# Kernel tuning notes

Measured on AMD Instinct MI355X. Metric: run time of the kernel, lower is better.

## Reference

```python
import jax, jax.numpy as jnp
import numpy as np

B, CIN, COUT, H, W = 4, 256, 256, 64, 64
K, G = 3, 4
PAD = (K - 1) // 2


def setup_inputs() -> dict:
    key = jax.random.key(0)
    k0, k1, k2, k3 = jax.random.split(key, 4)
    x = jax.random.normal(k0, (B, CIN, H, W), jnp.float32)
    y = jax.random.normal(k1, (B, 2, H, W), jnp.float32)
    # conv_offset: 1x1 conv, no bias, init std=0.1 (normal_init)
    w_offset = jax.random.normal(k2, (G * 2 * K * K, 2, 1, 1), jnp.float32) * 0.1
    # DeformConv2d weight, no bias, init std=0.01
    w_deform = jax.random.normal(k3, (COUT, CIN, K, K), jnp.float32) * 0.01
    return {"x": x, "y": y, "w_offset": w_offset, "w_deform": w_deform}


def _deform_conv(x, offset, weight):
    """DCN v1: stride 1, dilation 1, zero padding PAD, deform_groups=G, groups=1."""
    KK = K * K
    # mmcv offset layout: [B, G*2*KK, H, W] -> per group, per kernel pos, (dy, dx)
    off = offset.reshape(B, G, KK, 2, H, W)
    dy, dx = off[:, :, :, 0], off[:, :, :, 1]            # [B,G,KK,H,W]
    ii, jj = jnp.meshgrid(jnp.arange(K), jnp.arange(K), indexing="ij")
    ky = ii.reshape(KK).astype(x.dtype)                  # kernel row offsets
    kx = jj.reshape(KK).astype(x.dtype)                  # kernel col offsets
    base_y = jnp.arange(H, dtype=x.dtype)[None, :, None] - PAD + ky[:, None, None]  # [KK,H,1]
    base_x = jnp.arange(W, dtype=x.dtype)[None, None, :] - PAD + kx[:, None, None]  # [KK,1,W]
    yc = dy + base_y                                     # [B,G,KK,H,W]
    xc = dx + base_x

    Cg = CIN // G
    xg = x.reshape(B, G, Cg, H, W)

    def sample(xg1, yc1, xc1):
        # xg1 [Cg,H,W]; yc1/xc1 [KK,H,W] -> bilinear sample with zero padding
        y0 = jnp.floor(yc1)
        x0 = jnp.floor(xc1)
        wy = yc1 - y0
        wx = xc1 - x0
        y0i = y0.astype(jnp.int32)
        x0i = x0.astype(jnp.int32)

        def gather(yi, xi):
            valid = (yi >= 0) & (yi < H) & (xi >= 0) & (xi < W)
            v = xg1[:, jnp.clip(yi, 0, H - 1), jnp.clip(xi, 0, W - 1)]  # [Cg,KK,H,W]
            return v * valid[None].astype(xg1.dtype)

        v00 = gather(y0i, x0i)
        v01 = gather(y0i, x0i + 1)
        v10 = gather(y0i + 1, x0i)
        v11 = gather(y0i + 1, x0i + 1)
        return (v00 * (1 - wy) * (1 - wx) + v01 * (1 - wy) * wx
                + v10 * wy * (1 - wx) + v11 * wy * wx)

    sampled = jax.vmap(jax.vmap(sample))(xg, yc, xc)     # [B,G,Cg,KK,H,W]
    sampled = sampled.reshape(B, CIN, KK, H, W)
    wflat = weight.reshape(COUT, CIN, KK)
    return jnp.einsum("bckhw,ock->bohw", sampled, wflat)  # [B,COUT,H,W]


def reference(x, y, w_offset, w_deform):
    # offset = conv_offset(y.detach()), a 1x1 conv without bias
    y_det = jax.lax.stop_gradient(y)
    offset = jnp.einsum("bihw,oi->bohw", y_det, w_offset[:, :, 0, 0])
    out = _deform_conv(x, offset, w_deform)
    return jax.nn.relu(out)
```

## Files before the change

### kernel.cpp

```cpp
#include <hip/hip_runtime.h>
#include <cstddef>

#define B_    4
#define CIN_  256
#define COUT_ 256
#define H_    64
#define W_    64
#define KK_   9
#define G_    4
#define NSL   36
#define PW    80
#define PH    80
#define PADO  8

typedef short bf16x8 __attribute__((ext_vector_type(8)));
typedef float f32x4  __attribute__((ext_vector_type(4)));
typedef __attribute__((address_space(1))) const unsigned int* gptr_t;
typedef __attribute__((address_space(3))) unsigned int*       lptr_t;

__device__ __forceinline__ unsigned short f2bf(float v) {
    unsigned int u = __float_as_uint(v);
    u += 0x7fffu + ((u >> 16) & 1u);
    return (unsigned short)(u >> 16);
}
__device__ __forceinline__ float f_lo(unsigned int u) { return __uint_as_float(u << 16); }
__device__ __forceinline__ float f_hi(unsigned int u) { return __uint_as_float(u & 0xffff0000u); }

__global__ __launch_bounds__(256) void prep_kernel(const float* __restrict__ x,
                                                   unsigned short* __restrict__ xTp,
                                                   const float* __restrict__ w,
                                                   unsigned short* __restrict__ wb) {
    const int tid = threadIdx.x;
    if (blockIdx.x < 512) {
        __shared__ unsigned short s[128][66];
        const int bh    = blockIdx.x >> 1;
        const int chalf = blockIdx.x & 1;
        const int b     = bh >> 6, h = bh & 63;
        const size_t src_base = ((size_t)b * CIN_ + chalf * 128) * (H_ * W_) + h * W_;
        #pragma unroll 4
        for (int k = 0; k < 32; ++k) {
            int i = k * 256 + tid;
            int c = i >> 6, ww = i & 63;
            s[c][ww] = f2bf(x[src_base + (size_t)c * (H_ * W_) + ww]);
        }
        __syncthreads();
        const size_t dst_row = ((size_t)b * PH + (h + PADO)) * PW;
        #pragma unroll 4
        for (int k = 0; k < 20; ++k) {
            int j  = k * 256 + tid;
            int c2 = (j & 63) * 2, wp = j >> 6;
            unsigned int v = 0;
            if (wp >= PADO && wp < PADO + W_) {
                int ww = wp - PADO;
                v = (unsigned int)s[c2][ww] | ((unsigned int)s[c2 + 1][ww] << 16);
            }
            *(unsigned int*)(xTp + (dst_row + wp) * 256 + chalf * 128 + c2) = v;
        }
    } else if (blockIdx.x < 576) {
        const int bidx = blockIdx.x - 512;
        const int b = bidx >> 4, rr = bidx & 15;
        const int yp = (rr < PADO) ? rr : (PH - 16 + rr);
        unsigned short* dst = xTp + ((size_t)b * PH + yp) * PW * 256;
        #pragma unroll
        for (int k = 0; k < 10; ++k) {
            *(uint4*)(dst + (size_t)(k * 256 + tid) * 8) = make_uint4(0, 0, 0, 0);
        }
    } else {
        int idx = (blockIdx.x - 576) * 256 + tid;
        int e   = idx & 7;
        int pos = (idx >> 3) & 7;
        int o   = (idx >> 6) & 255;
        int t   = idx >> 14;
        int g   = t / 9, kk = t - g * 9;
        int j   = pos ^ (o & 7);
        int c   = g * 64 + j * 8 + e;
        wb[idx] = f2bf(w[(o * CIN_ + c) * KK_ + kk]);
    }
}

__global__ __launch_bounds__(1024, 4) void dcn_kernel(
    const unsigned short* __restrict__ xTp, const float* __restrict__ y,
    const float* __restrict__ w_off, const unsigned short* __restrict__ wb,
    float* __restrict__ out)
{
    __shared__ unsigned short s_W[3][COUT_ * 64];
    __shared__ unsigned short s_S[2][64 * 64];

    const int tid = threadIdx.x;
    const int bid = blockIdx.x;
    const int xcd = bid & 7;
    const int b   = xcd >> 1;
    const int h   = (xcd & 1) * 32 + (bid >> 3);

    const int sp = tid >> 4;
    const int c4 = tid & 15;

    const float yv0 = y[((b * 2 + 0) * H_ + h) * W_ + sp];
    const float yv1 = y[((b * 2 + 1) * H_ + h) * W_ + sp];
    const float spf = (float)(sp - 1 + PADO);
    const float hpf = (float)(h - 1 + PADO);

    const int lane = tid & 63, wave = tid >> 6;
    const int pg  = wave & 1, oh = wave >> 1;
    const int l15 = lane & 15, kq = lane >> 4, sw = l15 & 7;

    f32x4 acc[4];
    #pragma unroll
    for (int i = 0; i < 4; ++i) acc[i] = (f32x4){0.f, 0.f, 0.f, 0.f};

    const unsigned short* xb = xTp + (size_t)b * (PH * PW * 256) + c4 * 4;

    float w00, w01, w10, w11;
    uint2 A, Bv, C, D;

#define ISSUE_SAMPLE(t) do {                                                   \
    const int g_ = (t) / 9, kk_ = (t) % 9;                                     \
    const float4 co = *(const float4*)(w_off + (t) * 4);                       \
    const float dy = fmaf(yv0, co.x, yv1 * co.y);                              \
    const float dx = fmaf(yv0, co.z, yv1 * co.w);                              \
    const float yc = hpf + (float)(kk_ / 3) + dy;                              \
    const float xc = spf + (float)(kk_ % 3) + dx;                              \
    const float yf = floorf(yc), xf = floorf(xc);                              \
    const float wy = yc - yf,    wx = xc - xf;                                 \
    const int   yi = (int)yf,    xi = (int)xf;         \
    const float omy = 1.f - wy,  omx = 1.f - wx;                               \
    w00 = omy * omx;  w01 = omy * wx;                                          \
    w10 = wy * omx;   w11 = wy * wx;                                           \
    const int idx0 = (yi * PW + xi) * 256 + g_ * 64;               \
    A  = *(const uint2*)(xb + idx0);                                           \
    Bv = *(const uint2*)(xb + idx0 + 256);                 \
    C  = *(const uint2*)(xb + idx0 + PW * 256);                       \
    D  = *(const uint2*)(xb + idx0 + PW * 256 + 256);                          \
} while (0)

#define STAGE_W(t, buf) do {                                                   \
    const unsigned short* src = wb + (size_t)(t) * 16384;                      \
    _Pragma("unroll")                                                          \
    for (int j = 0; j < 2; ++j) {                                              \
        const int off = (j * 1024 + tid) * 8;                                  \
        __builtin_amdgcn_global_load_lds((gptr_t)(src + off),                  \
                                         (lptr_t)(s_W[buf] + off), 16, 0, 2); \
    }                                                                          \
} while (0)

#define WRITE_SAMPLE(buf) do {                                                 \
    float r0 = w00 * f_lo(A.x);                                                \
    r0 = fmaf(w01, f_lo(Bv.x), r0);                                            \
    r0 = fmaf(w10, f_lo(C.x),  r0);                                            \
    r0 = fmaf(w11, f_lo(D.x),  r0);                                            \
    float r1 = w00 * f_hi(A.x);                                                \
    r1 = fmaf(w01, f_hi(Bv.x), r1);                                            \
    r1 = fmaf(w10, f_hi(C.x),  r1);                                            \
    r1 = fmaf(w11, f_hi(D.x),  r1);                                            \
    float r2 = w00 * f_lo(A.y);                                                \
    r2 = fmaf(w01, f_lo(Bv.y), r2);                                            \
    r2 = fmaf(w10, f_lo(C.y),  r2);                                            \
    r2 = fmaf(w11, f_lo(D.y),  r2);                                            \
    float r3 = w00 * f_hi(A.y);                                                \
    r3 = fmaf(w01, f_hi(Bv.y), r3);                                            \
    r3 = fmaf(w10, f_hi(C.y),  r3);                                            \
    r3 = fmaf(w11, f_hi(D.y),  r3);                                            \
    unsigned int res0 = __builtin_amdgcn_perm(__float_as_uint(r1),             \
                                __float_as_uint(r0), 0x07060302u);             \
    unsigned int res1 = __builtin_amdgcn_perm(__float_as_uint(r3),             \
                                __float_as_uint(r2), 0x07060302u);             \
    *(uint2*)(s_S[buf] + sp * 64 + (((c4 >> 1) ^ (sp & 7)) * 8) +              \
              (c4 & 1) * 4) = make_uint2(res0, res1);                          \
} while (0)

#define MFMA_STEP(wb_, sb_) do {                                               \
    bf16x8 bf[2][2], af[2][2];                                                 \
    _Pragma("unroll")                                                          \
    for (int kh = 0; kh < 2; ++kh) {                                           \
        const int pos = ((kh * 4 + kq) ^ sw) * 8;                              \
        _Pragma("unroll")                                                      \
        for (int nt = 0; nt < 2; ++nt)                                         \
            bf[kh][nt] = *(const bf16x8*)(s_S[sb_] +                           \
                              (pg * 32 + nt * 16 + l15) * 64 + pos);           \
        _Pragma("unroll")                                                      \
        for (int mt = 0; mt < 2; ++mt)                                         \
            af[kh][mt] = *(const bf16x8*)(s_W[wb_] +                           \
                              (oh * 32 + mt * 16 + l15) * 64 + pos);           \
    }                                                                          \
    __builtin_amdgcn_s_setprio(1);                                             \
    _Pragma("unroll")                                                          \
    for (int kh = 0; kh < 2; ++kh)                                             \
        _Pragma("unroll")                                                      \
        for (int nt = 0; nt < 2; ++nt)                                         \
            _Pragma("unroll")                                                  \
            for (int mt = 0; mt < 2; ++mt)                                     \
                acc[nt * 2 + mt] = __builtin_amdgcn_mfma_f32_16x16x32_bf16(    \
                    af[kh][mt], bf[kh][nt], acc[nt * 2 + mt], 0, 0, 0);        \
    __builtin_amdgcn_s_setprio(0);                                             \
} while (0)

#define STEP(s_, WCUR, WPRE, SCUR, SNXT, DO_ISS, DO_STG, DO_BAR) do {          \
    if (DO_ISS) ISSUE_SAMPLE((s_) + 1);                                        \
    __builtin_amdgcn_sched_barrier(0);                                         \
    if (DO_STG) STAGE_W((s_) + 2, WPRE);                                       \
    __builtin_amdgcn_sched_barrier(0);                                         \
    MFMA_STEP(WCUR, SCUR);                                                     \
    __builtin_amdgcn_sched_barrier(0);                                         \
    if (DO_ISS) WRITE_SAMPLE(SNXT);                                            \
    __builtin_amdgcn_sched_barrier(0);                                         \
    if (DO_BAR) {                                                              \
        asm volatile("s_waitcnt lgkmcnt(0)" ::: "memory");                     \
        __builtin_amdgcn_sched_barrier(0);                                     \
        __builtin_amdgcn_s_barrier();                                          \
        __builtin_amdgcn_sched_barrier(0);                                     \
    }                                                                          \
} while (0)

    ISSUE_SAMPLE(0);
    __builtin_amdgcn_sched_barrier(0);
    STAGE_W(0, 0);
    __builtin_amdgcn_sched_barrier(0);
    WRITE_SAMPLE(0);
    __builtin_amdgcn_sched_barrier(0);
    STAGE_W(1, 1);
    __builtin_amdgcn_sched_barrier(0);
    asm volatile("s_waitcnt vmcnt(2) lgkmcnt(0)" ::: "memory");
    __builtin_amdgcn_sched_barrier(0);
    __builtin_amdgcn_s_barrier();
    __builtin_amdgcn_sched_barrier(0);

    for (int sb = 0; sb < 30; sb += 6) {
        STEP(sb + 0, 0, 2, 0, 1, 1, 1, 1);
        STEP(sb + 1, 1, 0, 1, 0, 1, 1, 1);
        STEP(sb + 2, 2, 1, 0, 1, 1, 1, 1);
        STEP(sb + 3, 0, 2, 1, 0, 1, 1, 1);
        STEP(sb + 4, 1, 0, 0, 1, 1, 1, 1);
        STEP(sb + 5, 2, 1, 1, 0, 1, 1, 1);
    }
    STEP(30, 0, 2, 0, 1, 1, 1, 1);
    STEP(31, 1, 0, 1, 0, 1, 1, 1);
    STEP(32, 2, 1, 0, 1, 1, 1, 1);
    STEP(33, 0, 2, 1, 0, 1, 1, 1);
    STEP(34, 1, 0, 0, 1, 1, 0, 1);
    STEP(35, 2, 1, 1, 0, 0, 0, 0);

    #pragma unroll
    for (int nt = 0; nt < 2; ++nt) {
        const int px = pg * 32 + nt * 16 + l15;
        #pragma unroll
        for (int mt = 0; mt < 2; ++mt) {
            const int obase = oh * 32 + mt * 16 + kq * 4;
            #pragma unroll
            for (int rr = 0; rr < 4; ++rr) {
                out[(((size_t)b * COUT_ + obase + rr) * H_ + h) * W_ + px] =
                    fmaxf(acc[nt * 2 + mt][rr], 0.f);
            }
        }
    }
#undef ISSUE_SAMPLE
#undef STAGE_W
#undef WRITE_SAMPLE
#undef MFMA_STEP
#undef STEP
}

extern "C" void kernel_launch(void* const* d_in, const int* in_sizes, int n_in,
                              void* d_out, int out_size, void* d_ws, size_t ws_size,
                              hipStream_t stream) {
    const float* x     = (const float*)d_in[0];
    const float* y     = (const float*)d_in[1];
    const float* w_off = (const float*)d_in[2];
    const float* w_def = (const float*)d_in[3];
    float* out = (float*)d_out;

    unsigned short* xTp = (unsigned short*)d_ws;
    unsigned short* wb  = (unsigned short*)d_ws + (size_t)B_ * PH * PW * 256;

    prep_kernel<<<2880, 256, 0, stream>>>(x, xTp, w_def, wb);
    dcn_kernel<<<256, 1024, 0, stream>>>(xTp, y, w_off, wb, out);
}
```

Measured before the change: 141.4 us.

## Halve block size, widen per-thread work, and prefetch samples two steps ahead

The DCN kernel moves from 1024 to 512 threads per block. Each thread now gathers 8 channels with 16-byte loads instead of 4 with 8-byte loads, and each wave computes 64 output channels (8 accumulators) instead of 32. Bilinear sample gathers are double-buffered in registers and issued two steps ahead, with a partial vmcnt wait so global loads overlap the MFMA work. The aim is to hide gather latency and get more MFMA per LDS fragment load, at the cost of more registers and fewer waves to hide latency.

```diff
diff --git a/kernel.cpp b/kernel.cpp
--- a/kernel.cpp
+++ b/kernel.cpp
@@ -78,7 +78,7 @@
     }
 }
 
-__global__ __launch_bounds__(1024, 4) void dcn_kernel(
+__global__ __launch_bounds__(512, 2) void dcn_kernel(
     const unsigned short* __restrict__ xTp, const float* __restrict__ y,
     const float* __restrict__ w_off, const unsigned short* __restrict__ wb,
     float* __restrict__ out)
@@ -92,8 +92,8 @@
     const int b   = xcd >> 1;
     const int h   = (xcd & 1) * 32 + (bid >> 3);
 
-    const int sp = tid >> 4;
-    const int c4 = tid & 15;
+    const int sp = tid >> 3;
+    const int c8 = tid & 7;
 
     const float yv0 = y[((b * 2 + 0) * H_ + h) * W_ + sp];
     const float yv1 = y[((b * 2 + 1) * H_ + h) * W_ + sp];
@@ -104,16 +104,16 @@
     const int pg  = wave & 1, oh = wave >> 1;
     const int l15 = lane & 15, kq = lane >> 4, sw = l15 & 7;
 
-    f32x4 acc[4];
+    f32x4 acc[8];
     #pragma unroll
-    for (int i = 0; i < 4; ++i) acc[i] = (f32x4){0.f, 0.f, 0.f, 0.f};
-
-    const unsigned short* xb = xTp + (size_t)b * (PH * PW * 256) + c4 * 4;
-
-    float w00, w01, w10, w11;
-    uint2 A, Bv, C, D;
-
-#define ISSUE_SAMPLE(t) do {                                                   \
+    for (int i = 0; i < 8; ++i) acc[i] = (f32x4){0.f, 0.f, 0.f, 0.f};
+
+    const unsigned short* xb = xTp + (size_t)b * (PH * PW * 256) + c8 * 8;
+
+    float w00[2], w01[2], w10[2], w11[2];
+    uint4 A[2], Bv[2], C[2], D[2];
+
+#define ISSUE_SAMPLE(t, P) do {                                                \
     const int g_ = (t) / 9, kk_ = (t) % 9;                                     \
     const float4 co = *(const float4*)(w_off + (t) * 4);                       \
     const float dy = fmaf(yv0, co.x, yv1 * co.y);                              \
@@ -124,52 +124,50 @@
     const float wy = yc - yf,    wx = xc - xf;                                 \
     const int   yi = (int)yf,    xi = (int)xf;         \
     const float omy = 1.f - wy,  omx = 1.f - wx;                               \
-    w00 = omy * omx;  w01 = omy * wx;                                          \
-    w10 = wy * omx;   w11 = wy * wx;                                           \
+    w00[P] = omy * omx;  w01[P] = omy * wx;                                    \
+    w10[P] = wy * omx;   w11[P] = wy * wx;                                     \
     const int idx0 = (yi * PW + xi) * 256 + g_ * 64;               \
-    A  = *(const uint2*)(xb + idx0);                                           \
-    Bv = *(const uint2*)(xb + idx0 + 256);                 \
-    C  = *(const uint2*)(xb + idx0 + PW * 256);                       \
-    D  = *(const uint2*)(xb + idx0 + PW * 256 + 256);                          \
+    A[P]  = *(const uint4*)(xb + idx0);                                        \
+    Bv[P] = *(const uint4*)(xb + idx0 + 256);                                  \
+    C[P]  = *(const uint4*)(xb + idx0 + PW * 256);                             \
+    D[P]  = *(const uint4*)(xb + idx0 + PW * 256 + 256);                       \
 } while (0)
 
 #define STAGE_W(t, buf) do {                                                   \
     const unsigned short* src = wb + (size_t)(t) * 16384;                      \
     _Pragma("unroll")                                                          \
-    for (int j = 0; j < 2; ++j) {                                              \
-        const int off = (j * 1024 + tid) * 8;                                  \
+    for (int j = 0; j < 4; ++j) {                                              \
+        const int off = (j * 512 + tid) * 8;                                   \
         __builtin_amdgcn_global_load_lds((gptr_t)(src + off),                  \
                                          (lptr_t)(s_W[buf] + off), 16, 0, 2); \
     }                                                                          \
 } while (0)
 
-#define WRITE_SAMPLE(buf) do {                                                 \
-    float r0 = w00 * f_lo(A.x);                                                \
-    r0 = fmaf(w01, f_lo(Bv.x), r0);                                            \
-    r0 = fmaf(w10, f_lo(C.x),  r0);                                            \
-    r0 = fmaf(w11, f_lo(D.x),  r0);                                            \
-    float r1 = w00 * f_hi(A.x);                                                \
-    r1 = fmaf(w01, f_hi(Bv.x), r1);                                            \
-    r1 = fmaf(w10, f_hi(C.x),  r1);                                            \
-    r1 = fmaf(w11, f_hi(D.x),  r1);                                            \
-    float r2 = w00 * f_lo(A.y);                                                \
-    r2 = fmaf(w01, f_lo(Bv.y), r2);                                            \
-    r2 = fmaf(w10, f_lo(C.y),  r2);                                            \
-    r2 = fmaf(w11, f_lo(D.y),  r2);                                            \
-    float r3 = w00 * f_hi(A.y);                                                \
-    r3 = fmaf(w01, f_hi(Bv.y), r3);                                            \
-    r3 = fmaf(w10, f_hi(C.y),  r3);                                            \
-    r3 = fmaf(w11, f_hi(D.y),  r3);                                            \
-    unsigned int res0 = __builtin_amdgcn_perm(__float_as_uint(r1),             \
-                                __float_as_uint(r0), 0x07060302u);             \
-    unsigned int res1 = __builtin_amdgcn_perm(__float_as_uint(r3),             \
-                                __float_as_uint(r2), 0x07060302u);             \
-    *(uint2*)(s_S[buf] + sp * 64 + (((c4 >> 1) ^ (sp & 7)) * 8) +              \
-              (c4 & 1) * 4) = make_uint2(res0, res1);                          \
+#define WRITE_SAMPLE(P, buf) do {                                              \
+    const unsigned int av[4] = {A[P].x, A[P].y, A[P].z, A[P].w};               \
+    const unsigned int bv[4] = {Bv[P].x, Bv[P].y, Bv[P].z, Bv[P].w};           \
+    const unsigned int cv[4] = {C[P].x, C[P].y, C[P].z, C[P].w};               \
+    const unsigned int dv[4] = {D[P].x, D[P].y, D[P].z, D[P].w};               \
+    unsigned int res[4];                                                       \
+    _Pragma("unroll")                                                          \
+    for (int q = 0; q < 4; ++q) {                                              \
+        float rl = w00[P] * f_lo(av[q]);                                       \
+        rl = fmaf(w01[P], f_lo(bv[q]), rl);                                    \
+        rl = fmaf(w10[P], f_lo(cv[q]), rl);                                    \
+        rl = fmaf(w11[P], f_lo(dv[q]), rl);                                    \
+        float rh = w00[P] * f_hi(av[q]);                                       \
+        rh = fmaf(w01[P], f_hi(bv[q]), rh);                                    \
+        rh = fmaf(w10[P], f_hi(cv[q]), rh);                                    \
+        rh = fmaf(w11[P], f_hi(dv[q]), rh);                                    \
+        res[q] = __builtin_amdgcn_perm(__float_as_uint(rh),                    \
+                                       __float_as_uint(rl), 0x07060302u);      \
+    }                                                                          \
+    *(uint4*)(s_S[buf] + sp * 64 + ((c8 ^ (sp & 7)) * 8)) =                    \
+        make_uint4(res[0], res[1], res[2], res[3]);                            \
 } while (0)
 
 #define MFMA_STEP(wb_, sb_) do {                                               \
-    bf16x8 bf[2][2], af[2][2];                                                 \
+    bf16x8 bf[2][2], af[2][4];                                                 \
     _Pragma("unroll")                                                          \
     for (int kh = 0; kh < 2; ++kh) {                                           \
         const int pos = ((kh * 4 + kq) ^ sw) * 8;                              \
@@ -178,9 +176,9 @@
             bf[kh][nt] = *(const bf16x8*)(s_S[sb_] +                           \
                               (pg * 32 + nt * 16 + l15) * 64 + pos);           \
         _Pragma("unroll")                                                      \
-        for (int mt = 0; mt < 2; ++mt)                                         \
+        for (int mt = 0; mt < 4; ++mt)                                         \
             af[kh][mt] = *(const bf16x8*)(s_W[wb_] +                           \
-                              (oh * 32 + mt * 16 + l15) * 64 + pos);           \
+                              (oh * 64 + mt * 16 + l15) * 64 + pos);           \
     }                                                                          \
     __builtin_amdgcn_s_setprio(1);                                             \
     _Pragma("unroll")                                                          \
@@ -188,67 +186,68 @@
         _Pragma("unroll")                                                      \
         for (int nt = 0; nt < 2; ++nt)                                         \
             _Pragma("unroll")                                                  \
-            for (int mt = 0; mt < 2; ++mt)                                     \
-                acc[nt * 2 + mt] = __builtin_amdgcn_mfma_f32_16x16x32_bf16(    \
-                    af[kh][mt], bf[kh][nt], acc[nt * 2 + mt], 0, 0, 0);        \
+            for (int mt = 0; mt < 4; ++mt)                                     \
+                acc[nt * 4 + mt] = __builtin_amdgcn_mfma_f32_16x16x32_bf16(    \
+                    af[kh][mt], bf[kh][nt], acc[nt * 4 + mt], 0, 0, 0);        \
     __builtin_amdgcn_s_setprio(0);                                             \
 } while (0)
 
-#define STEP(s_, WCUR, WPRE, SCUR, SNXT, DO_ISS, DO_STG, DO_BAR) do {          \
-    if (DO_ISS) ISSUE_SAMPLE((s_) + 1);                                        \
-    __builtin_amdgcn_sched_barrier(0);                                         \
-    if (DO_STG) STAGE_W((s_) + 2, WPRE);                                       \
+#define STEP(s_, WCUR, WPRE, SCUR, SNXT, PiS, PwR, DO_PF, END8) do {           \
+    if (DO_PF) ISSUE_SAMPLE((s_) + 2, PiS);                                    \
+    __builtin_amdgcn_sched_barrier(0);                                         \
+    if (DO_PF) STAGE_W((s_) + 2, WPRE);                                        \
     __builtin_amdgcn_sched_barrier(0);                                         \
     MFMA_STEP(WCUR, SCUR);                                                     \
     __builtin_amdgcn_sched_barrier(0);                                         \
-    if (DO_ISS) WRITE_SAMPLE(SNXT);                                            \
-    __builtin_amdgcn_sched_barrier(0);                                         \
-    if (DO_BAR) {                                                              \
-        asm volatile("s_waitcnt lgkmcnt(0)" ::: "memory");                     \
-        __builtin_amdgcn_sched_barrier(0);                                     \
-        __builtin_amdgcn_s_barrier();                                          \
-        __builtin_amdgcn_sched_barrier(0);                                     \
-    }                                                                          \
-} while (0)
-
-    ISSUE_SAMPLE(0);
+    WRITE_SAMPLE(PwR, SNXT);                                                   \
+    __builtin_amdgcn_sched_barrier(0);                                         \
+    if (END8) asm volatile("s_waitcnt vmcnt(8) lgkmcnt(0)" ::: "memory");      \
+    else      asm volatile("s_waitcnt vmcnt(0) lgkmcnt(0)" ::: "memory");      \
+    __builtin_amdgcn_sched_barrier(0);                                         \
+    __builtin_amdgcn_s_barrier();                                              \
+    __builtin_amdgcn_sched_barrier(0);                                         \
+} while (0)
+
+    ISSUE_SAMPLE(0, 0);
     __builtin_amdgcn_sched_barrier(0);
     STAGE_W(0, 0);
     __builtin_amdgcn_sched_barrier(0);
-    WRITE_SAMPLE(0);
+    ISSUE_SAMPLE(1, 1);
     __builtin_amdgcn_sched_barrier(0);
     STAGE_W(1, 1);
     __builtin_amdgcn_sched_barrier(0);
-    asm volatile("s_waitcnt vmcnt(2) lgkmcnt(0)" ::: "memory");
+    WRITE_SAMPLE(0, 0);
+    __builtin_amdgcn_sched_barrier(0);
+    asm volatile("s_waitcnt vmcnt(8) lgkmcnt(0)" ::: "memory");
     __builtin_amdgcn_sched_barrier(0);
     __builtin_amdgcn_s_barrier();
     __builtin_amdgcn_sched_barrier(0);
 
     for (int sb = 0; sb < 30; sb += 6) {
-        STEP(sb + 0, 0, 2, 0, 1, 1, 1, 1);
-        STEP(sb + 1, 1, 0, 1, 0, 1, 1, 1);
-        STEP(sb + 2, 2, 1, 0, 1, 1, 1, 1);
-        STEP(sb + 3, 0, 2, 1, 0, 1, 1, 1);
-        STEP(sb + 4, 1, 0, 0, 1, 1, 1, 1);
-        STEP(sb + 5, 2, 1, 1, 0, 1, 1, 1);
+        STEP(sb + 0, 0, 2, 0, 1, 0, 1, 1, 1);
+        STEP(sb + 1, 1, 0, 1, 0, 1, 0, 1, 1);
+        STEP(sb + 2, 2, 1, 0, 1, 0, 1, 1, 1);
+        STEP(sb + 3, 0, 2, 1, 0, 1, 0, 1, 1);
+        STEP(sb + 4, 1, 0, 0, 1, 0, 1, 1, 1);
+        STEP(sb + 5, 2, 1, 1, 0, 1, 0, 1, 1);
     }
-    STEP(30, 0, 2, 0, 1, 1, 1, 1);
-    STEP(31, 1, 0, 1, 0, 1, 1, 1);
-    STEP(32, 2, 1, 0, 1, 1, 1, 1);
-    STEP(33, 0, 2, 1, 0, 1, 1, 1);
-    STEP(34, 1, 0, 0, 1, 1, 0, 1);
-    STEP(35, 2, 1, 1, 0, 0, 0, 0);
+    STEP(30, 0, 2, 0, 1, 0, 1, 1, 1);
+    STEP(31, 1, 0, 1, 0, 1, 0, 1, 1);
+    STEP(32, 2, 1, 0, 1, 0, 1, 1, 1);
+    STEP(33, 0, 2, 1, 0, 1, 0, 1, 1);
+    STEP(34, 1, 0, 0, 1, 0, 1, 0, 0);
+    MFMA_STEP(2, 1);
 
     #pragma unroll
     for (int nt = 0; nt < 2; ++nt) {
         const int px = pg * 32 + nt * 16 + l15;
         #pragma unroll
-        for (int mt = 0; mt < 2; ++mt) {
-            const int obase = oh * 32 + mt * 16 + kq * 4;
+        for (int mt = 0; mt < 4; ++mt) {
+            const int obase = oh * 64 + mt * 16 + kq * 4;
             #pragma unroll
             for (int rr = 0; rr < 4; ++rr) {
                 out[(((size_t)b * COUT_ + obase + rr) * H_ + h) * W_ + px] =
-                    fmaxf(acc[nt * 2 + mt][rr], 0.f);
+                    fmaxf(acc[nt * 4 + mt][rr], 0.f);
             }
         }
     }
@@ -272,5 +271,5 @@
     unsigned short* wb  = (unsigned short*)d_ws + (size_t)B_ * PH * PW * 256;
 
     prep_kernel<<<2880, 256, 0, stream>>>(x, xTp, w_def, wb);
-    dcn_kernel<<<256, 1024, 0, stream>>>(xTp, y, w_off, wb, out);
-}
+    dcn_kernel<<<256, 512, 0, stream>>>(xTp, y, w_off, wb, out);
+}
```

Measured after the change: 132.6 us. 6.2% less time.
